# Kernel optimization log

Hardware: AMD Instinct MI355X
Metric: run time of the kernel (lower is better)

## Reference

```python
import jax, jax.numpy as jnp
import numpy as np

B, L, D, H = 4, 2048, 1024, 16
HD = D // H


def setup_inputs() -> dict:
    key = jax.random.key(0)
    ks = jax.random.split(key, 12)
    s = 1.0 / np.sqrt(D)
    return {
        "q": jax.random.normal(ks[0], (B, L, D), jnp.float32),
        "k": jax.random.normal(ks[1], (B, L, D), jnp.float32),
        "v": jax.random.normal(ks[2], (B, L, D), jnp.float32),
        "mask": jax.random.randint(ks[3], (1, 1, L, L), 0, 2, jnp.int32),
        "Wq": jax.random.normal(ks[4], (D, D), jnp.float32) * s,
        "bq": jnp.zeros((D,), jnp.float32),
        "Wk": jax.random.normal(ks[5], (D, D), jnp.float32) * s,
        "bk": jnp.zeros((D,), jnp.float32),
        "Wv": jax.random.normal(ks[6], (D, D), jnp.float32) * s,
        "bv": jnp.zeros((D,), jnp.float32),
        "Wo": jax.random.normal(ks[7], (D, D), jnp.float32) * s,
        "bo": jnp.zeros((D,), jnp.float32),
    }


def _split_heads(x):
    # (B, L, D) -> (B, H, L, HD)
    b, l, _ = x.shape
    return x.reshape(b, l, H, HD).transpose(0, 2, 1, 3)


def reference(q, k, v, mask, Wq, bq, Wk, bk, Wv, bv, Wo, bo):
    qw = q @ Wq.T + bq
    kw = k @ Wk.T + bk
    vw = v @ Wv.T + bv
    qh, kh, vh = _split_heads(qw), _split_heads(kw), _split_heads(vw)
    scale = 1.0 / jnp.sqrt(jnp.float32(HD))
    scores = jnp.einsum('bhqd,bhkd->bhqk', qh, kh) * scale
    scores = scores + mask.astype(scores.dtype) * (-1e15)
    weights = jax.nn.softmax(scores, axis=-1)
    attn = jnp.einsum('bhqk,bhkd->bhqd', weights, vh)  # (B, H, L, HD)
    attn = attn.transpose(0, 2, 1, 3).reshape(q.shape[0], q.shape[1], D)
    return attn @ Wo.T + bo
```

## Files before the change

kernel.cpp:

```cpp
#include <hip/hip_runtime.h>
#include <stdint.h>

#define B_ 4
#define L_ 2048
#define D_ 1024
#define H_ 16
#define HD_ 64

typedef __attribute__((ext_vector_type(8))) short short8;
typedef __attribute__((ext_vector_type(4))) float f32x4;

__device__ __forceinline__ unsigned short f2bf(float f) {
  union { float f; unsigned int u; } x; x.f = f;
  unsigned int u = x.u;
  u += 0x7FFFu + ((u >> 16) & 1u);
  return (unsigned short)(u >> 16);
}

__device__ __forceinline__ f32x4 zero4() {
  f32x4 z; z[0] = 0.f; z[1] = 0.f; z[2] = 0.f; z[3] = 0.f; return z;
}

__device__ __forceinline__ void gload_lds16(const unsigned short* gp, unsigned short* lp) {
  __builtin_amdgcn_global_load_lds(
      (const __attribute__((address_space(1))) unsigned int*)(const void*)gp,
      (__attribute__((address_space(3))) unsigned int*)(void*)lp, 16, 0, 0);
}

__global__ __launch_bounds__(256) void cast4_bf16(
    const float* __restrict__ s0, const float* __restrict__ s1,
    const float* __restrict__ s2, const float* __restrict__ s3,
    unsigned short* __restrict__ d0, unsigned short* __restrict__ d1,
    unsigned short* __restrict__ d2, unsigned short* __restrict__ d3, int n) {
  int w = blockIdx.y;
  const float* src = (w == 0) ? s0 : (w == 1) ? s1 : (w == 2) ? s2 : s3;
  unsigned short* dst = (w == 0) ? d0 : (w == 1) ? d1 : (w == 2) ? d2 : d3;
  int stride = gridDim.x * blockDim.x * 4;
  for (int i = (blockIdx.x * blockDim.x + threadIdx.x) * 4; i < n; i += stride) {
    float4 f = *(const float4*)(src + i);
    uint2 o;
    o.x = (unsigned int)f2bf(f.x) | ((unsigned int)f2bf(f.y) << 16);
    o.y = (unsigned int)f2bf(f.z) | ((unsigned int)f2bf(f.w) << 16);
    *(uint2*)(dst + i) = o;
  }
}

__global__ __launch_bounds__(256) void mask_pack2(const int* __restrict__ m,
                                                  unsigned long long* __restrict__ words) {
  int wid = blockIdx.x * 4 + (threadIdx.x >> 6);
  int lane = threadIdx.x & 63;
  int qt = wid >> 5, kt = wid & 31;
  int q = qt * 16 + (lane & 15);
  int g = lane >> 4;
  #pragma unroll
  for (int w = 0; w < 16; ++w) {
    int nt = w >> 2, r = w & 3;
    int key = kt * 64 + nt * 16 + g * 4 + r;
    unsigned long long bal = __ballot(m[(size_t)q * L_ + key] != 0);
    if (lane == 0) words[((size_t)qt * 32 + kt) * 16 + w] = bal;
  }
}

template<int MODE, bool AF32, bool FUSE2>
__global__ __launch_bounds__(256) void gemm_bt(
    const void* __restrict__ A0v, const void* __restrict__ A1v,
    const unsigned short* __restrict__ B0w, const unsigned short* __restrict__ B1w,
    const float* __restrict__ bias0, const float* __restrict__ bias1,
    void* __restrict__ C0p, void* __restrict__ C1p,
    float scale0, float scale1, int K)
{
  __shared__ __align__(16) unsigned short As[128 * 64];
  __shared__ __align__(16) unsigned short Bs[128 * 64];
  __shared__ __align__(16) unsigned short Tsh[MODE == 2 ? 64 * 136 : 16];
  const int t = threadIdx.x;
  const int lane = t & 63;
  const int wave = t >> 6;
  const int g = lane >> 4, cl = lane & 15;
  const int wm = wave >> 1, wn = wave & 1;

  const int bx = blockIdx.x;
  const int by = blockIdx.y;
  const int bz = FUSE2 ? blockIdx.z : 0;

  const void* Av = (FUSE2 && bz) ? A1v : A0v;
  const unsigned short* Bw = (FUSE2 && bz) ? B1w : B0w;
  const float* bias = (FUSE2 && bz) ? bias1 : bias0;
  void* Cp = (FUSE2 && bz) ? C1p : C0p;
  const float scale = (FUSE2 && bz) ? scale1 : scale0;

  const int m0 = bx * 128, n0 = by * 128;

  f32x4 acc[4][4];
  #pragma unroll
  for (int i = 0; i < 4; ++i)
    #pragma unroll
    for (int j = 0; j < 4; ++j) acc[i][j] = zero4();

  for (int k0 = 0; k0 < K; k0 += 64) {
    __syncthreads();
    #pragma unroll
    for (int i = 0; i < 4; ++i) {
      int c = i * 256 + t;
      int row = c >> 3, cc = c & 7;
      int scc = ((cc ^ (row & 7)) << 3);
      if constexpr (AF32) {
        const float* Af = (const float*)Av;
        const float* ap = Af + (size_t)(m0 + row) * K + k0 + cc * 8;
        float4 f0 = *(const float4*)ap;
        float4 f1 = *(const float4*)(ap + 4);
        unsigned int u0, u1, u2, u3;
        asm("v_cvt_pk_bf16_f32 %0, %1, %2" : "=v"(u0) : "v"(f0.x), "v"(f0.y));
        asm("v_cvt_pk_bf16_f32 %0, %1, %2" : "=v"(u1) : "v"(f0.z), "v"(f0.w));
        asm("v_cvt_pk_bf16_f32 %0, %1, %2" : "=v"(u2) : "v"(f1.x), "v"(f1.y));
        asm("v_cvt_pk_bf16_f32 %0, %1, %2" : "=v"(u3) : "v"(f1.z), "v"(f1.w));
        uint4 u; u.x = u0; u.y = u1; u.z = u2; u.w = u3;
        *(uint4*)&As[row * 64 + scc] = u;
      } else {
        gload_lds16((const unsigned short*)Av + (size_t)(m0 + row) * K + k0 + scc,
                    &As[c << 3]);
      }
      gload_lds16(Bw + (size_t)(n0 + row) * K + k0 + scc, &Bs[c << 3]);
    }
    __syncthreads();
    #pragma unroll
    for (int kk = 0; kk < 2; ++kk) {
      short8 af[4], bf[4];
      #pragma unroll
      for (int mt = 0; mt < 4; ++mt)
        af[mt] = *(const short8*)&As[(wm * 64 + mt * 16 + cl) * 64
                                     + ((kk * 32 + g * 8) ^ ((cl & 7) << 3))];
      #pragma unroll
      for (int nt = 0; nt < 4; ++nt)
        bf[nt] = *(const short8*)&Bs[(wn * 64 + nt * 16 + cl) * 64
                                     + ((kk * 32 + g * 8) ^ ((cl & 7) << 3))];
      #pragma unroll
      for (int mt = 0; mt < 4; ++mt)
        #pragma unroll
        for (int nt = 0; nt < 4; ++nt)
          acc[mt][nt] = __builtin_amdgcn_mfma_f32_16x16x32_bf16(af[mt], bf[nt], acc[mt][nt], 0, 0, 0);
    }
  }

  if constexpr (MODE <= 1) {
    #pragma unroll
    for (int nt = 0; nt < 4; ++nt) {
      int col = n0 + wn * 64 + nt * 16 + cl;
      float bv = bias[col];
      #pragma unroll
      for (int mt = 0; mt < 4; ++mt) {
        #pragma unroll
        for (int r = 0; r < 4; ++r) {
          int row = m0 + wm * 64 + mt * 16 + g * 4 + r;
          float val = (acc[mt][nt][r] + bv) * scale;
          if (MODE == 0)
            ((float*)Cp)[(size_t)row * D_ + col] = val;
          else
            ((unsigned short*)Cp)[(size_t)row * D_ + col] = f2bf(val);
        }
      }
    }
  } else {
    const int b = m0 >> 11;
    #pragma unroll 1
    for (int half = 0; half < 2; ++half) {
      __syncthreads();
      if (wn == half) {
        #pragma unroll
        for (int nt = 0; nt < 4; ++nt) {
          float bv = bias[n0 + wn * 64 + nt * 16 + cl];
          #pragma unroll
          for (int mt = 0; mt < 4; ++mt) {
            float v0 = acc[mt][nt][0] + bv, v1 = acc[mt][nt][1] + bv;
            float v2 = acc[mt][nt][2] + bv, v3 = acc[mt][nt][3] + bv;
            unsigned int lo, hi;
            asm("v_cvt_pk_bf16_f32 %0, %1, %2" : "=v"(lo) : "v"(v0), "v"(v1));
            asm("v_cvt_pk_bf16_f32 %0, %1, %2" : "=v"(hi) : "v"(v2), "v"(v3));
            uint2 u; u.x = lo; u.y = hi;
            *(uint2*)&Tsh[(nt * 16 + cl) * 136 + wm * 64 + mt * 16 + g * 4] = u;
          }
        }
      }
      __syncthreads();
      #pragma unroll
      for (int p = 0; p < 4; ++p) {
        int chunk = p * 256 + t;
        int c = chunk >> 4, li = (chunk & 15) * 8;
        int colg = n0 + half * 64 + c;
        int hh = colg >> 6, d = colg & 63;
        short8 vv = *(const short8*)&Tsh[c * 136 + li];
        *(short8*)((unsigned short*)Cp + (((size_t)(b * 16 + hh)) << 17)
                   + (size_t)d * L_ + (m0 & (L_ - 1)) + li) = vv;
      }
    }
  }
}

__global__ __launch_bounds__(256) void flash_attn(
    const unsigned short* __restrict__ qw,
    const unsigned short* __restrict__ kw,
    const unsigned short* __restrict__ vt,
    const unsigned long long* __restrict__ mwords,
    unsigned short* __restrict__ ctx)
{
  __shared__ __align__(16) unsigned short Ksh[2][64 * 64];
  __shared__ __align__(16) unsigned short Vsh[2][64 * 64];
  __shared__ __align__(16) unsigned short Psh[64 * 64];

  const int t = threadIdx.x;
  const int lane = t & 63;
  const int wave = t >> 6;
  const int g = lane >> 4, cl = lane & 15;
  const int bh = blockIdx.y;
  const int b = bh >> 4, h = bh & 15;
  const int qb = blockIdx.x * 64 + wave * 16;

  const size_t baseq = (size_t)b * L_ * D_ + (size_t)h * HD_;
  const size_t basev = (size_t)bh * HD_ * L_;

  const int qtu = __builtin_amdgcn_readfirstlane(blockIdx.x * 4 + wave);
  const unsigned long long* __restrict__ mrow = mwords + (size_t)qtu * (32 * 16);

  const int c0 = t, c1 = 256 + t;
  const int r0 = c0 >> 3, r1 = c1 >> 3;
  const int s0 = ((c0 & 7) ^ (r0 & 7)) << 3, s1 = ((c1 & 7) ^ (r1 & 7)) << 3;
  const unsigned short* kg0 = kw + baseq + (size_t)r0 * D_ + s0;
  const unsigned short* kg1 = kw + baseq + (size_t)r1 * D_ + s1;
  const unsigned short* vg0 = vt + basev + (size_t)r0 * L_ + s0;
  const unsigned short* vg1 = vt + basev + (size_t)r1 * L_ + s1;

#define STAGE_KV(bufi, kti)                                                     \
  {                                                                             \
    const size_t ko = (size_t)(kti) * (64 * D_);                                \
    const int vo = (kti) * 64;                                                  \
    gload_lds16(kg0 + ko, &Ksh[bufi][c0 << 3]);                                 \
    gload_lds16(vg0 + vo, &Vsh[bufi][c0 << 3]);                                 \
    gload_lds16(kg1 + ko, &Ksh[bufi][c1 << 3]);                                 \
    gload_lds16(vg1 + vo, &Vsh[bufi][c1 << 3]);                                 \
  }

  short8 bq[2];
  #pragma unroll
  for (int kk = 0; kk < 2; ++kk)
    bq[kk] = *(const short8*)(qw + baseq + (size_t)(qb + cl) * D_ + kk * 32 + g * 8);

  short8 ones;
  #pragma unroll
  for (int i = 0; i < 8; ++i) ones[i] = (short)0x3F80;

  f32x4 oacc[4], lsum;
  #pragma unroll
  for (int dt = 0; dt < 4; ++dt) oacc[dt] = zero4();
  lsum = zero4();
  float ninf = -1e30f;

  STAGE_KV(0, 0);
  __syncthreads();

  int buf = 0;
  for (int kt = 0; kt < L_ / 64; ++kt) {
    unsigned long long Mw[16];
    #pragma unroll
    for (int w = 0; w < 16; ++w) Mw[w] = mrow[kt * 16 + w];

    if (kt + 1 < L_ / 64) STAGE_KV(buf ^ 1, kt + 1);

    f32x4 sc[4];
    #pragma unroll
    for (int nt = 0; nt < 4; ++nt) {
      sc[nt][0] = -16.f; sc[nt][1] = -16.f; sc[nt][2] = -16.f; sc[nt][3] = -16.f;
    }
    __builtin_amdgcn_s_setprio(1);
    #pragma unroll
    for (int kk = 0; kk < 2; ++kk) {
      #pragma unroll
      for (int nt = 0; nt < 4; ++nt) {
        short8 ak = *(const short8*)&Ksh[buf][(nt * 16 + cl) * 64
                                             + ((kk * 32 + g * 8) ^ ((cl & 7) << 3))];
        sc[nt] = __builtin_amdgcn_mfma_f32_16x16x32_bf16(ak, bq[kk], sc[nt], 0, 0, 0);
      }
    }
    __builtin_amdgcn_s_setprio(0);

    float p[4][4];
    #pragma unroll
    for (int nt = 0; nt < 4; ++nt)
      #pragma unroll
      for (int r = 0; r < 4; ++r) {
        float sv;
        asm("v_cndmask_b32 %0, %1, %2, %3"
            : "=v"(sv)
            : "v"(sc[nt][r]), "v"(ninf), "s"(Mw[nt * 4 + r]));
        p[nt][r] = __builtin_amdgcn_exp2f(sv);
      }

    #pragma unroll
    for (int nt = 0; nt < 4; ++nt) {
      unsigned int lo, hi;
      asm("v_cvt_pk_bf16_f32 %0, %1, %2" : "=v"(lo) : "v"(p[nt][0]), "v"(p[nt][1]));
      asm("v_cvt_pk_bf16_f32 %0, %1, %2" : "=v"(hi) : "v"(p[nt][2]), "v"(p[nt][3]));
      uint2 u; u.x = lo; u.y = hi;
      *(uint2*)&Psh[(((wave * 16 + cl) * 64) + nt * 16 + g * 4) ^ ((cl & 7) << 3)] = u;
    }

    short8 pa[2];
    #pragma unroll
    for (int kk = 0; kk < 2; ++kk)
      pa[kk] = *(const short8*)&Psh[(((wave * 16 + cl) * 64) + kk * 32 + g * 8)
                                    ^ ((cl & 7) << 3)];
    __builtin_amdgcn_s_setprio(1);
    #pragma unroll
    for (int kk = 0; kk < 2; ++kk) {
      #pragma unroll
      for (int dt = 0; dt < 4; ++dt) {
        short8 bv = *(const short8*)&Vsh[buf][(dt * 16 + cl) * 64
                                             + ((kk * 32 + g * 8) ^ ((cl & 7) << 3))];
        oacc[dt] = __builtin_amdgcn_mfma_f32_16x16x32_bf16(pa[kk], bv, oacc[dt], 0, 0, 0);
      }
      lsum = __builtin_amdgcn_mfma_f32_16x16x32_bf16(pa[kk], ones, lsum, 0, 0, 0);
    }
    __builtin_amdgcn_s_setprio(0);

    __syncthreads();
    buf ^= 1;
  }

  #pragma unroll
  for (int r = 0; r < 4; ++r) {
    float iv = __builtin_amdgcn_rcpf(lsum[r]);
    #pragma unroll
    for (int dt = 0; dt < 4; ++dt)
      ctx[baseq + (size_t)(qb + g * 4 + r) * D_ + dt * 16 + cl] = f2bf(oacc[dt][r] * iv);
  }
#undef STAGE_KV
}

extern "C" void kernel_launch(void* const* d_in, const int* in_sizes, int n_in,
                              void* d_out, int out_size, void* d_ws, size_t ws_size,
                              hipStream_t stream) {
  (void)in_sizes; (void)n_in; (void)out_size; (void)ws_size;
  const float* q    = (const float*)d_in[0];
  const float* k    = (const float*)d_in[1];
  const float* v    = (const float*)d_in[2];
  const int*   mask = (const int*)d_in[3];
  const float* Wq   = (const float*)d_in[4];
  const float* bq   = (const float*)d_in[5];
  const float* Wk   = (const float*)d_in[6];
  const float* bk   = (const float*)d_in[7];
  const float* Wv   = (const float*)d_in[8];
  const float* bv   = (const float*)d_in[9];
  const float* Wo   = (const float*)d_in[10];
  const float* bo   = (const float*)d_in[11];

  char* ws = (char*)d_ws;
  const size_t MB = 1024 * 1024;
  unsigned short* Wqb  = (unsigned short*)(ws + 16 * MB);
  unsigned short* Wkb  = (unsigned short*)(ws + 18 * MB);
  unsigned short* Wvb  = (unsigned short*)(ws + 20 * MB);
  unsigned short* Wob  = (unsigned short*)(ws + 22 * MB);
  unsigned short* qwb  = (unsigned short*)(ws + 24 * MB);
  unsigned short* kwb  = (unsigned short*)(ws + 40 * MB);
  unsigned short* vtb  = (unsigned short*)(ws + 56 * MB);
  unsigned short* ctx  = (unsigned short*)(ws + 72 * MB);
  unsigned long long* mwd = (unsigned long long*)(ws + 88 * MB);

  const int NW = D_ * D_;

  cast4_bf16<<<dim3(512, 4), 256, 0, stream>>>(Wq, Wk, Wv, Wo, Wqb, Wkb, Wvb, Wob, NW);
  mask_pack2<<<1024, 256, 0, stream>>>(mask, mwd);

  dim3 gproj(64, 8);
  dim3 gproj2(64, 8, 2);

  const float QSCALE = 0.125f * 1.44269504088896340736f;

  gemm_bt<1, true, true><<<gproj2, 256, 0, stream>>>(
      q, k, Wqb, Wkb, bq, bk, qwb, kwb, QSCALE, 1.0f, D_);
  gemm_bt<2, true, false><<<gproj, 256, 0, stream>>>(
      v, v, Wvb, Wvb, bv, bv, vtb, vtb, 1.0f, 1.0f, D_);

  flash_attn<<<dim3(L_ / 64, B_ * H_), 256, 0, stream>>>(qwb, kwb, vtb, mwd, ctx);

  gemm_bt<0, false, false><<<gproj, 256, 0, stream>>>(
      ctx, ctx, Wob, Wob, bo, bo, d_out, d_out, 1.0f, 1.0f, D_);
}
```

Baseline: 242.5 us.

## Fuse Q/K/V projections into one launch and remap attention grid for locality

Merges the separate QK projection and V projection GEMM launches into one three-way batched kernel, so the V transpose epilogue reuses the shared A/B buffer instead of holding an extra Tsh allocation. The output GEMM becomes its own specialized kernel. Flash attention moves to a 1D grid whose block index is remapped so that groups of 8 heads sharing the same query tile run together, which is meant to improve cache reuse of the mask words and K/V. Expected gains are fewer launches, better wave fill, and lower shared memory use, at the cost of runtime branching on blockIdx.z.

```diff
diff --git a/kernel.cpp b/kernel.cpp
--- a/kernel.cpp
+++ b/kernel.cpp
@@ -61,34 +61,30 @@
   }
 }
 
-template<int MODE, bool AF32, bool FUSE2>
-__global__ __launch_bounds__(256) void gemm_bt(
-    const void* __restrict__ A0v, const void* __restrict__ A1v,
-    const unsigned short* __restrict__ B0w, const unsigned short* __restrict__ B1w,
-    const float* __restrict__ bias0, const float* __restrict__ bias1,
-    void* __restrict__ C0p, void* __restrict__ C1p,
-    float scale0, float scale1, int K)
+__global__ __launch_bounds__(256) void gemm_proj3(
+    const float* __restrict__ Aq, const float* __restrict__ Ak, const float* __restrict__ Avv,
+    const unsigned short* __restrict__ Bq, const unsigned short* __restrict__ Bk,
+    const unsigned short* __restrict__ Bv,
+    const float* __restrict__ bqv, const float* __restrict__ bkv, const float* __restrict__ bvv,
+    unsigned short* __restrict__ Cq, unsigned short* __restrict__ Ck,
+    unsigned short* __restrict__ Cv,
+    float qscale, int K)
 {
-  __shared__ __align__(16) unsigned short As[128 * 64];
-  __shared__ __align__(16) unsigned short Bs[128 * 64];
-  __shared__ __align__(16) unsigned short Tsh[MODE == 2 ? 64 * 136 : 16];
+  __shared__ __align__(16) unsigned short Sh[2 * 128 * 64];
+  unsigned short* As = Sh;
+  unsigned short* Bs = Sh + 128 * 64;
   const int t = threadIdx.x;
   const int lane = t & 63;
   const int wave = t >> 6;
   const int g = lane >> 4, cl = lane & 15;
   const int wm = wave >> 1, wn = wave & 1;
-
-  const int bx = blockIdx.x;
-  const int by = blockIdx.y;
-  const int bz = FUSE2 ? blockIdx.z : 0;
-
-  const void* Av = (FUSE2 && bz) ? A1v : A0v;
-  const unsigned short* Bw = (FUSE2 && bz) ? B1w : B0w;
-  const float* bias = (FUSE2 && bz) ? bias1 : bias0;
-  void* Cp = (FUSE2 && bz) ? C1p : C0p;
-  const float scale = (FUSE2 && bz) ? scale1 : scale0;
-
-  const int m0 = bx * 128, n0 = by * 128;
+  const int bz = blockIdx.z;
+  const int m0 = blockIdx.x * 128, n0 = blockIdx.y * 128;
+
+  const float* Af = (bz == 0) ? Aq : (bz == 1) ? Ak : Avv;
+  const unsigned short* Bw = (bz == 0) ? Bq : (bz == 1) ? Bk : Bv;
+  const float* bias = (bz == 0) ? bqv : (bz == 1) ? bkv : bvv;
+  const float scale = (bz == 0) ? qscale : 1.0f;
 
   f32x4 acc[4][4];
   #pragma unroll
@@ -103,22 +99,16 @@
       int c = i * 256 + t;
       int row = c >> 3, cc = c & 7;
       int scc = ((cc ^ (row & 7)) << 3);
-      if constexpr (AF32) {
-        const float* Af = (const float*)Av;
-        const float* ap = Af + (size_t)(m0 + row) * K + k0 + cc * 8;
-        float4 f0 = *(const float4*)ap;
-        float4 f1 = *(const float4*)(ap + 4);
-        unsigned int u0, u1, u2, u3;
-        asm("v_cvt_pk_bf16_f32 %0, %1, %2" : "=v"(u0) : "v"(f0.x), "v"(f0.y));
-        asm("v_cvt_pk_bf16_f32 %0, %1, %2" : "=v"(u1) : "v"(f0.z), "v"(f0.w));
-        asm("v_cvt_pk_bf16_f32 %0, %1, %2" : "=v"(u2) : "v"(f1.x), "v"(f1.y));
-        asm("v_cvt_pk_bf16_f32 %0, %1, %2" : "=v"(u3) : "v"(f1.z), "v"(f1.w));
-        uint4 u; u.x = u0; u.y = u1; u.z = u2; u.w = u3;
-        *(uint4*)&As[row * 64 + scc] = u;
-      } else {
-        gload_lds16((const unsigned short*)Av + (size_t)(m0 + row) * K + k0 + scc,
-                    &As[c << 3]);
-      }
+      const float* ap = Af + (size_t)(m0 + row) * K + k0 + cc * 8;
+      float4 f0 = *(const float4*)ap;
+      float4 f1 = *(const float4*)(ap + 4);
+      unsigned int u0, u1, u2, u3;
+      asm("v_cvt_pk_bf16_f32 %0, %1, %2" : "=v"(u0) : "v"(f0.x), "v"(f0.y));
+      asm("v_cvt_pk_bf16_f32 %0, %1, %2" : "=v"(u1) : "v"(f0.z), "v"(f0.w));
+      asm("v_cvt_pk_bf16_f32 %0, %1, %2" : "=v"(u2) : "v"(f1.x), "v"(f1.y));
+      asm("v_cvt_pk_bf16_f32 %0, %1, %2" : "=v"(u3) : "v"(f1.z), "v"(f1.w));
+      uint4 u; u.x = u0; u.y = u1; u.z = u2; u.w = u3;
+      *(uint4*)&As[row * 64 + scc] = u;
       gload_lds16(Bw + (size_t)(n0 + row) * K + k0 + scc, &Bs[c << 3]);
     }
     __syncthreads();
@@ -141,7 +131,8 @@
     }
   }
 
-  if constexpr (MODE <= 1) {
+  if (bz < 2) {
+    unsigned short* Cp = (bz == 0) ? Cq : Ck;
     #pragma unroll
     for (int nt = 0; nt < 4; ++nt) {
       int col = n0 + wn * 64 + nt * 16 + cl;
@@ -151,15 +142,12 @@
         #pragma unroll
         for (int r = 0; r < 4; ++r) {
           int row = m0 + wm * 64 + mt * 16 + g * 4 + r;
-          float val = (acc[mt][nt][r] + bv) * scale;
-          if (MODE == 0)
-            ((float*)Cp)[(size_t)row * D_ + col] = val;
-          else
-            ((unsigned short*)Cp)[(size_t)row * D_ + col] = f2bf(val);
+          Cp[(size_t)row * D_ + col] = f2bf((acc[mt][nt][r] + bv) * scale);
         }
       }
     }
   } else {
+    unsigned short* Tsh = Sh;
     const int b = m0 >> 11;
     #pragma unroll 1
     for (int half = 0; half < 2; ++half) {
@@ -188,8 +176,74 @@
         int colg = n0 + half * 64 + c;
         int hh = colg >> 6, d = colg & 63;
         short8 vv = *(const short8*)&Tsh[c * 136 + li];
-        *(short8*)((unsigned short*)Cp + (((size_t)(b * 16 + hh)) << 17)
+        *(short8*)(Cv + (((size_t)(b * 16 + hh)) << 17)
                    + (size_t)d * L_ + (m0 & (L_ - 1)) + li) = vv;
+      }
+    }
+  }
+}
+
+__global__ __launch_bounds__(256) void gemm_out(
+    const unsigned short* __restrict__ A,
+    const unsigned short* __restrict__ Bw,
+    const float* __restrict__ bias,
+    float* __restrict__ Cp, int K)
+{
+  __shared__ __align__(16) unsigned short As[128 * 64];
+  __shared__ __align__(16) unsigned short Bs[128 * 64];
+  const int t = threadIdx.x;
+  const int lane = t & 63;
+  const int wave = t >> 6;
+  const int g = lane >> 4, cl = lane & 15;
+  const int wm = wave >> 1, wn = wave & 1;
+  const int m0 = blockIdx.x * 128, n0 = blockIdx.y * 128;
+
+  f32x4 acc[4][4];
+  #pragma unroll
+  for (int i = 0; i < 4; ++i)
+    #pragma unroll
+    for (int j = 0; j < 4; ++j) acc[i][j] = zero4();
+
+  for (int k0 = 0; k0 < K; k0 += 64) {
+    __syncthreads();
+    #pragma unroll
+    for (int i = 0; i < 4; ++i) {
+      int c = i * 256 + t;
+      int row = c >> 3, cc = c & 7;
+      int scc = ((cc ^ (row & 7)) << 3);
+      gload_lds16(A + (size_t)(m0 + row) * K + k0 + scc, &As[c << 3]);
+      gload_lds16(Bw + (size_t)(n0 + row) * K + k0 + scc, &Bs[c << 3]);
+    }
+    __syncthreads();
+    #pragma unroll
+    for (int kk = 0; kk < 2; ++kk) {
+      short8 af[4], bf[4];
+      #pragma unroll
+      for (int mt = 0; mt < 4; ++mt)
+        af[mt] = *(const short8*)&As[(wm * 64 + mt * 16 + cl) * 64
+                                     + ((kk * 32 + g * 8) ^ ((cl & 7) << 3))];
+      #pragma unroll
+      for (int nt = 0; nt < 4; ++nt)
+        bf[nt] = *(const short8*)&Bs[(wn * 64 + nt * 16 + cl) * 64
+                                     + ((kk * 32 + g * 8) ^ ((cl & 7) << 3))];
+      #pragma unroll
+      for (int mt = 0; mt < 4; ++mt)
+        #pragma unroll
+        for (int nt = 0; nt < 4; ++nt)
+          acc[mt][nt] = __builtin_amdgcn_mfma_f32_16x16x32_bf16(af[mt], bf[nt], acc[mt][nt], 0, 0, 0);
+    }
+  }
+
+  #pragma unroll
+  for (int nt = 0; nt < 4; ++nt) {
+    int col = n0 + wn * 64 + nt * 16 + cl;
+    float bv = bias[col];
+    #pragma unroll
+    for (int mt = 0; mt < 4; ++mt) {
+      #pragma unroll
+      for (int r = 0; r < 4; ++r) {
+        int row = m0 + wm * 64 + mt * 16 + g * 4 + r;
+        Cp[(size_t)row * D_ + col] = acc[mt][nt][r] + bv;
       }
     }
   }
@@ -210,14 +264,17 @@
   const int lane = t & 63;
   const int wave = t >> 6;
   const int g = lane >> 4, cl = lane & 15;
-  const int bh = blockIdx.y;
+
+  const int d0i = blockIdx.x;
+  const int xq = (d0i >> 3) & 31;
+  const int bh = (d0i & 7) + ((d0i >> 8) << 3);
   const int b = bh >> 4, h = bh & 15;
-  const int qb = blockIdx.x * 64 + wave * 16;
+  const int qb = xq * 64 + wave * 16;
 
   const size_t baseq = (size_t)b * L_ * D_ + (size_t)h * HD_;
   const size_t basev = (size_t)bh * HD_ * L_;
 
-  const int qtu = __builtin_amdgcn_readfirstlane(blockIdx.x * 4 + wave);
+  const int qtu = __builtin_amdgcn_readfirstlane(xq * 4 + wave);
   const unsigned long long* __restrict__ mrow = mwords + (size_t)qtu * (32 * 16);
 
   const int c0 = t, c1 = 256 + t;
@@ -368,18 +425,12 @@
   cast4_bf16<<<dim3(512, 4), 256, 0, stream>>>(Wq, Wk, Wv, Wo, Wqb, Wkb, Wvb, Wob, NW);
   mask_pack2<<<1024, 256, 0, stream>>>(mask, mwd);
 
-  dim3 gproj(64, 8);
-  dim3 gproj2(64, 8, 2);
-
   const float QSCALE = 0.125f * 1.44269504088896340736f;
 
-  gemm_bt<1, true, true><<<gproj2, 256, 0, stream>>>(
-      q, k, Wqb, Wkb, bq, bk, qwb, kwb, QSCALE, 1.0f, D_);
-  gemm_bt<2, true, false><<<gproj, 256, 0, stream>>>(
-      v, v, Wvb, Wvb, bv, bv, vtb, vtb, 1.0f, 1.0f, D_);
-
-  flash_attn<<<dim3(L_ / 64, B_ * H_), 256, 0, stream>>>(qwb, kwb, vtb, mwd, ctx);
-
-  gemm_bt<0, false, false><<<gproj, 256, 0, stream>>>(
-      ctx, ctx, Wob, Wob, bo, bo, d_out, d_out, 1.0f, 1.0f, D_);
-}
+  gemm_proj3<<<dim3(64, 8, 3), 256, 0, stream>>>(
+      q, k, v, Wqb, Wkb, Wvb, bq, bk, bv, qwb, kwb, vtb, QSCALE, D_);
+
+  flash_attn<<<dim3(2048), 256, 0, stream>>>(qwb, kwb, vtb, mwd, ctx);
+
+  gemm_out<<<dim3(64, 8), 256, 0, stream>>>(ctx, Wob, bo, (float*)d_out, D_);
+}
```

After: 267.8 us. 1.1x slower.
